# Kernel tuning notes

Measured on AMD Instinct MI355X. Metric: run time of the kernel, lower is better.

## Reference

```python
import jax, jax.numpy as jnp
import numpy as np

D = 1024  # q_dim == k_dim == v_dim
B, QL, KL = 8, 2048, 2048
NEG_BIG = -1e12  # matches torch masked_fill_(-1000000000000.0)


def setup_inputs() -> dict:
    key = jax.random.key(0)
    kq, kk, kv, kp = jax.random.split(key, 4)
    Q = jax.random.normal(kq, (B, QL, D), dtype=jnp.float32)
    K = jax.random.normal(kk, (B, KL, D), dtype=jnp.float32)
    V = jax.random.normal(kv, (B, KL, D), dtype=jnp.float32)
    attn_mask = jnp.zeros((QL, KL), dtype=jnp.float32)
    key_pad_mask = jax.random.randint(kp, (B, KL), 0, 2).astype(jnp.bool_)
    return {"Q": Q, "K": K, "V": V, "attn_mask": attn_mask, "key_pad_mask": key_pad_mask}


def reference(Q, K, V, attn_mask, key_pad_mask):
    temperature = jnp.asarray(np.sqrt(D), dtype=Q.dtype)
    # [B, QL, KL] scores: dot mode
    scores = jnp.einsum("bqd,bkd->bqk", Q, K) / temperature
    scores = scores + attn_mask[None, :, :]
    scores = jnp.where(key_pad_mask[:, None, :], NEG_BIG, scores)
    attn_weights = jax.nn.softmax(scores, axis=-1)  # dropout p=0 -> identity
    attn_ctx = jnp.einsum("bqk,bkd->bqd", attn_weights, V)
    return attn_ctx, attn_weights
```

## Files before the change

kernel.cpp:

```cpp
#include <hip/hip_runtime.h>
#include <hip/hip_fp16.h>

#define B_ 8
#define QL_ 2048
#define KL_ 2048
#define D_ 1024

typedef _Float16 f16x8 __attribute__((ext_vector_type(8)));
typedef _Float16 f16x4 __attribute__((ext_vector_type(4)));
typedef float f32x4 __attribute__((ext_vector_type(4)));

__device__ __forceinline__ void async16(const void* g, void* l) {
  __builtin_amdgcn_global_load_lds(
      (const __attribute__((address_space(1))) unsigned int*)g,
      (__attribute__((address_space(3))) unsigned int*)l, 16, 0, 0);
}

__global__ __launch_bounds__(256) void prep_k(const int* __restrict__ pad,
                                              int* __restrict__ pos,
                                              int* __restrict__ kcp) {
  const int b = blockIdx.x;
  const int t = threadIdx.x;
  const int lane = t & 63, wv = t >> 6;
  __shared__ int wsum[4], wpre[4], kc_sh;
  const int* pr = pad + b * KL_;
  int* po = pos + b * KL_;
  int c[8], loc = 0;
#pragma unroll
  for (int j = 0; j < 8; ++j) {
    c[j] = (pr[t * 8 + j] == 0);
    loc += c[j];
  }
  int inc = loc;
  for (int d = 1; d < 64; d <<= 1) {
    int v = __shfl_up(inc, d);
    if (lane >= d) inc += v;
  }
  if (lane == 63) wsum[wv] = inc;
  __syncthreads();
  if (t == 0) {
    int acc = 0;
    for (int w = 0; w < 4; ++w) {
      wpre[w] = acc;
      acc += wsum[w];
    }
    kc_sh = acc;
    kcp[b] = (acc == 0) ? KL_ : acc;
  }
  __syncthreads();
  const int kc = kc_sh;
  int base = wpre[wv] + inc - loc;
#pragma unroll
  for (int j = 0; j < 8; ++j) {
    po[t * 8 + j] = (kc == 0) ? (t * 8 + j) : base;
    base += c[j];
  }
}

__global__ __launch_bounds__(256) void cvt2_k(const float* __restrict__ Q,
                                              const float* __restrict__ K,
                                              _Float16* __restrict__ Qh,
                                              _Float16* __restrict__ Kh) {
  constexpr int HALF = B_ * QL_ * D_ / 8 / 256;
  const bool isQ = blockIdx.x < HALF;
  const int i = (isQ ? blockIdx.x : blockIdx.x - HALF) * 256 + threadIdx.x;
  const float4* src = reinterpret_cast<const float4*>(isQ ? Q : K);
  const float scale = isQ ? 0.03125f : 1.0f;
  float4 a = src[i * 2], b = src[i * 2 + 1];
  f16x8 h;
  h[0] = (_Float16)(a.x * scale); h[1] = (_Float16)(a.y * scale);
  h[2] = (_Float16)(a.z * scale); h[3] = (_Float16)(a.w * scale);
  h[4] = (_Float16)(b.x * scale); h[5] = (_Float16)(b.y * scale);
  h[6] = (_Float16)(b.z * scale); h[7] = (_Float16)(b.w * scale);
  reinterpret_cast<f16x8*>(isQ ? Qh : Kh)[i] = h;
}

__global__ __launch_bounds__(256) void vt_k(const float* __restrict__ V,
                                            _Float16* __restrict__ VT) {
  __shared__ float tile[32][33];
  const int k0 = blockIdx.x * 32, d0 = blockIdx.y * 32, b = blockIdx.z;
  const float* Vb = V + (size_t)b * KL_ * D_;
  _Float16* VTb = VT + (size_t)b * D_ * KL_;
  const int c = threadIdx.x & 31, r = threadIdx.x >> 5;
#pragma unroll
  for (int s = 0; s < 4; ++s)
    tile[r + s * 8][c] = Vb[(size_t)(k0 + r + s * 8) * D_ + d0 + c];
  __syncthreads();
#pragma unroll
  for (int s = 0; s < 4; ++s)
    VTb[(size_t)(d0 + r + s * 8) * KL_ + k0 + c] = (_Float16)tile[c][r + s * 8];
}

__global__ __launch_bounds__(256) void vtc_k(const float* __restrict__ V,
                                             _Float16* __restrict__ VTc,
                                             const int* __restrict__ pad,
                                             const int* __restrict__ pos) {
  __shared__ float tile[32][33];
  const int k0 = blockIdx.x * 32, d0 = blockIdx.y * 32, b = blockIdx.z;
  const float* Vb = V + (size_t)b * KL_ * D_;
  _Float16* VTb = VTc + (size_t)b * D_ * KL_;
  const int c = threadIdx.x & 31, r = threadIdx.x >> 5;
#pragma unroll
  for (int s = 0; s < 4; ++s)
    tile[r + s * 8][c] = Vb[(size_t)(k0 + r + s * 8) * D_ + d0 + c];
  __syncthreads();
  const int kk = k0 + c;
  const int keep = (pad[b * KL_ + kk] == 0);
  const int col = pos[b * KL_ + kk];
#pragma unroll
  for (int s = 0; s < 4; ++s)
    if (keep)
      VTb[(size_t)(d0 + r + s * 8) * KL_ + col] = (_Float16)tile[c][r + s * 8];
}

template <bool SCORES>
__global__ __launch_bounds__(512, 2) void fgemm_k(
    const _Float16* __restrict__ Ah, const _Float16* __restrict__ Bh,
    float* __restrict__ Cf, _Float16* __restrict__ Ch) {
  constexpr int Mc = 2048;
  constexpr int Nc = SCORES ? 2048 : 1024;
  constexpr int Kc = SCORES ? 1024 : 2048;
  constexpr int NIT = Kc / 64;
  constexpr int GX = Mc / 256, GY = Nc / 256;
  constexpr int CPX = B_ * GX * GY / 8;

  extern __shared__ char lds[];

  const int t = threadIdx.x;
  const int lane = t & 63;
  const int wid = t >> 6;
  const int wr = wid >> 2, wc = wid & 3;
  const int lo = lane & 15, hi = lane >> 4;

  const int id = blockIdx.x;
  const int swz = (id & 7) * CPX + (id >> 3);
  const int b = swz / (GX * GY);
  const int rem = swz % (GX * GY);
  const int m0 = (rem / GY) * 256, n0 = (rem % GY) * 256;

  const _Float16* Ab = Ah + (size_t)b * Mc * Kc;
  const _Float16* Bb = Bh + (size_t)b * Nc * Kc;

  int aoff[4], boff[4], ldst[4];
#pragma unroll
  for (int j = 0; j < 4; ++j) {
    const int row = j * 64 + wid * 8 + (lane >> 3);
    const int cg = (lane & 7) ^ (lane >> 3);
    aoff[j] = (m0 + row) * Kc + cg * 8;
    boff[j] = (n0 + row) * Kc + cg * 8;
    ldst[j] = j * 8192 + wid * 1024;
  }

  auto stage = [&](int it, int slot) {
    char* base = lds + slot * 65536;
    const int kb = it * 64;
#pragma unroll
    for (int j = 0; j < 4; ++j) {
      async16(Ab + aoff[j] + kb, base + ldst[j]);
      async16(Bb + boff[j] + kb, base + 32768 + ldst[j]);
    }
  };

  f32x4 acc[8][4];
#pragma unroll
  for (int m = 0; m < 8; ++m)
#pragma unroll
    for (int n = 0; n < 4; ++n)
#pragma unroll
      for (int i = 0; i < 4; ++i) acc[m][n][i] = 0.0f;

  int raf[8], rbf_[4];
#pragma unroll
  for (int m = 0; m < 8; ++m) {
    const int r = wr * 128 + m * 16 + lo;
    raf[m] = r * 128 + ((hi ^ (r & 7)) << 4);
  }
#pragma unroll
  for (int n = 0; n < 4; ++n) {
    const int r = wc * 64 + n * 16 + lo;
    rbf_[n] = r * 128 + ((hi ^ (r & 7)) << 4);
  }

  auto compute = [&](int slot) {
    const char* Ac = lds + slot * 65536;
    const char* Bc = Ac + 32768;
#pragma unroll
    for (int kh = 0; kh < 2; ++kh) {
      const int kx = kh * 64;
      f16x8 af[8], bfr[4];
#pragma unroll
      for (int m = 0; m < 8; ++m)
        af[m] = *reinterpret_cast<const f16x8*>(Ac + (raf[m] ^ kx));
#pragma unroll
      for (int n = 0; n < 4; ++n)
        bfr[n] = *reinterpret_cast<const f16x8*>(Bc + (rbf_[n] ^ kx));
      __builtin_amdgcn_s_setprio(1);
#pragma unroll
      for (int m = 0; m < 8; ++m)
#pragma unroll
        for (int n = 0; n < 4; ++n)
          acc[m][n] = __builtin_amdgcn_mfma_f32_16x16x32_f16(
              af[m], bfr[n], acc[m][n], 0, 0, 0);
      __builtin_amdgcn_s_setprio(0);
      __builtin_amdgcn_sched_barrier(0);
    }
  };

  stage(0, 0);
  for (int it = 0; it < NIT; ++it) {
    asm volatile("s_waitcnt vmcnt(0) lgkmcnt(0)" ::: "memory");
    __builtin_amdgcn_sched_barrier(0);
    __builtin_amdgcn_s_barrier();
    if (it + 1 < NIT) stage(it + 1, (it + 1) & 1);
    compute(it & 1);
  }

  if constexpr (SCORES) {
    _Float16* Cb = Ch + (size_t)b * Mc * Nc;
#pragma unroll
    for (int n = 0; n < 4; ++n) {
      const int col = n0 + wc * 64 + n * 16 + lo;
#pragma unroll
      for (int m = 0; m < 8; ++m) {
        const int r0 = m0 + wr * 128 + m * 16 + hi * 4;
#pragma unroll
        for (int i = 0; i < 4; ++i)
          Cb[(size_t)(r0 + i) * Nc + col] = (_Float16)acc[m][n][i];
      }
    }
  } else {
    float* Cb = Cf + (size_t)b * Mc * Nc;
#pragma unroll
    for (int n = 0; n < 4; ++n) {
      const int col = n0 + wc * 64 + n * 16 + lo;
#pragma unroll
      for (int m = 0; m < 8; ++m) {
        const int r0 = m0 + wr * 128 + m * 16 + hi * 4;
#pragma unroll
        for (int i = 0; i < 4; ++i)
          Cb[(size_t)(r0 + i) * Nc + col] = acc[m][n][i];
      }
    }
  }
}

__global__ __launch_bounds__(512, 2) void fgemm_pv(
    const _Float16* __restrict__ Whc, const _Float16* __restrict__ VTc,
    float* __restrict__ Cf, const int* __restrict__ kcp) {
  constexpr int Mc = 2048, Nc = 1024;
  constexpr int GX = 8, GY = 4;
  constexpr int CPX = B_ * GX * GY / 8;

  extern __shared__ char lds[];

  const int t = threadIdx.x;
  const int lane = t & 63;
  const int wid = t >> 6;
  const int wr = wid >> 2, wc = wid & 3;
  const int lo = lane & 15, hi = lane >> 4;

  const int id = blockIdx.x;
  const int swz = (id & 7) * CPX + (id >> 3);
  const int b = swz / (GX * GY);
  const int rem = swz % (GX * GY);
  const int m0 = (rem / GY) * 256, n0 = (rem % GY) * 256;

  const int kc = kcp[b];
  const int KA = (kc + 63) & ~63;
  const int NIT = KA >> 6;

  const _Float16* Ab = Whc + (size_t)b * 2048 * 2048;
  const _Float16* Bb = VTc + (size_t)b * Nc * KL_;

  int aoff[4], boff[4], ldst[4];
#pragma unroll
  for (int j = 0; j < 4; ++j) {
    const int row = j * 64 + wid * 8 + (lane >> 3);
    const int cg = (lane & 7) ^ (lane >> 3);
    aoff[j] = (m0 + row) * KA + cg * 8;
    boff[j] = (n0 + row) * KL_ + cg * 8;
    ldst[j] = j * 8192 + wid * 1024;
  }

  auto stage = [&](int it, int slot) {
    char* base = lds + slot * 65536;
    const int kb = it * 64;
#pragma unroll
    for (int j = 0; j < 4; ++j) {
      async16(Ab + aoff[j] + kb, base + ldst[j]);
      async16(Bb + boff[j] + kb, base + 32768 + ldst[j]);
    }
  };

  f32x4 acc[8][4];
#pragma unroll
  for (int m = 0; m < 8; ++m)
#pragma unroll
    for (int n = 0; n < 4; ++n)
#pragma unroll
      for (int i = 0; i < 4; ++i) acc[m][n][i] = 0.0f;

  int raf[8], rbf_[4];
#pragma unroll
  for (int m = 0; m < 8; ++m) {
    const int r = wr * 128 + m * 16 + lo;
    raf[m] = r * 128 + ((hi ^ (r & 7)) << 4);
  }
#pragma unroll
  for (int n = 0; n < 4; ++n) {
    const int r = wc * 64 + n * 16 + lo;
    rbf_[n] = r * 128 + ((hi ^ (r & 7)) << 4);
  }

  auto compute = [&](int slot) {
    const char* Ac = lds + slot * 65536;
    const char* Bc = Ac + 32768;
#pragma unroll
    for (int kh = 0; kh < 2; ++kh) {
      const int kx = kh * 64;
      f16x8 af[8], bfr[4];
#pragma unroll
      for (int m = 0; m < 8; ++m)
        af[m] = *reinterpret_cast<const f16x8*>(Ac + (raf[m] ^ kx));
#pragma unroll
      for (int n = 0; n < 4; ++n)
        bfr[n] = *reinterpret_cast<const f16x8*>(Bc + (rbf_[n] ^ kx));
      __builtin_amdgcn_s_setprio(1);
#pragma unroll
      for (int m = 0; m < 8; ++m)
#pragma unroll
        for (int n = 0; n < 4; ++n)
          acc[m][n] = __builtin_amdgcn_mfma_f32_16x16x32_f16(
              af[m], bfr[n], acc[m][n], 0, 0, 0);
      __builtin_amdgcn_s_setprio(0);
      __builtin_amdgcn_sched_barrier(0);
    }
  };

  stage(0, 0);
  for (int it = 0; it < NIT; ++it) {
    asm volatile("s_waitcnt vmcnt(0) lgkmcnt(0)" ::: "memory");
    __builtin_amdgcn_sched_barrier(0);
    __builtin_amdgcn_s_barrier();
    if (it + 1 < NIT) stage(it + 1, (it + 1) & 1);
    compute(it & 1);
  }

  float* Cb = Cf + (size_t)b * Mc * Nc;
#pragma unroll
  for (int n = 0; n < 4; ++n) {
    const int col = n0 + wc * 64 + n * 16 + lo;
#pragma unroll
    for (int m = 0; m < 8; ++m) {
      const int r0 = m0 + wr * 128 + m * 16 + hi * 4;
#pragma unroll
      for (int i = 0; i < 4; ++i)
        Cb[(size_t)(r0 + i) * Nc + col] = acc[m][n][i];
    }
  }
}

template <bool COMPACT>
__global__ __launch_bounds__(256) void softmax_k(
    const _Float16* __restrict__ Sh, float* __restrict__ W,
    _Float16* __restrict__ Wh, const float* __restrict__ mask,
    const int* __restrict__ pad, const int* __restrict__ pos,
    const int* __restrict__ kcp) {
  const int row = blockIdx.x * 4 + (threadIdx.x >> 6);
  const int lane = threadIdx.x & 63;
  const int b = row >> 11, q = row & 2047;
  const f16x4* Sr = reinterpret_cast<const f16x4*>(Sh + (size_t)row * KL_);
  float4* Wr = reinterpret_cast<float4*>(W + (size_t)row * KL_);
  const float4* Mr = reinterpret_cast<const float4*>(mask + (size_t)q * KL_);
  const int4* Pr = reinterpret_cast<const int4*>(pad + (size_t)b * KL_);
  int4 pk[8];
  float4 v[8];
#pragma unroll
  for (int s = 0; s < 8; ++s) {
    f16x4 sv = Sr[s * 64 + lane];
    float4 mk = Mr[s * 64 + lane];
    int4 p = Pr[s * 64 + lane];
    pk[s] = p;
    float4 x;
    x.x = p.x ? -1e12f : (float)sv[0] + mk.x;
    x.y = p.y ? -1e12f : (float)sv[1] + mk.y;
    x.z = p.z ? -1e12f : (float)sv[2] + mk.z;
    x.w = p.w ? -1e12f : (float)sv[3] + mk.w;
    v[s] = x;
  }
  float mx = -3.402823466e38f;
#pragma unroll
  for (int s = 0; s < 8; ++s)
    mx = fmaxf(mx, fmaxf(fmaxf(v[s].x, v[s].y), fmaxf(v[s].z, v[s].w)));
#pragma unroll
  for (int off = 32; off > 0; off >>= 1) mx = fmaxf(mx, __shfl_xor(mx, off));
  float sum = 0.0f;
#pragma unroll
  for (int s = 0; s < 8; ++s) {
    v[s].x = __expf(v[s].x - mx);
    v[s].y = __expf(v[s].y - mx);
    v[s].z = __expf(v[s].z - mx);
    v[s].w = __expf(v[s].w - mx);
    sum += v[s].x + v[s].y + v[s].z + v[s].w;
  }
#pragma unroll
  for (int off = 32; off > 0; off >>= 1) sum += __shfl_xor(sum, off);
  const float inv = 1.0f / sum;

  if constexpr (COMPACT) {
    const int kc = kcp[b];
    const int kcpad = (kc + 63) & ~63;
    _Float16* Wc = Wh + (size_t)b * 2048 * 2048 + (size_t)q * kcpad;
    const int4* Po = reinterpret_cast<const int4*>(pos + (size_t)b * KL_);
#pragma unroll
    for (int s = 0; s < 8; ++s) {
      float4 o;
      o.x = v[s].x * inv;
      o.y = v[s].y * inv;
      o.z = v[s].z * inv;
      o.w = v[s].w * inv;
      Wr[s * 64 + lane] = o;
      int4 ps = Po[s * 64 + lane];
      if (!pk[s].x) Wc[ps.x] = (_Float16)o.x;
      if (!pk[s].y) Wc[ps.y] = (_Float16)o.y;
      if (!pk[s].z) Wc[ps.z] = (_Float16)o.z;
      if (!pk[s].w) Wc[ps.w] = (_Float16)o.w;
    }
    if (kc + lane < kcpad) Wc[kc + lane] = (_Float16)0.0f;
  } else {
    f16x4* Whr = reinterpret_cast<f16x4*>(Wh + (size_t)row * KL_);
#pragma unroll
    for (int s = 0; s < 8; ++s) {
      float4 o;
      o.x = v[s].x * inv;
      o.y = v[s].y * inv;
      o.z = v[s].z * inv;
      o.w = v[s].w * inv;
      Wr[s * 64 + lane] = o;
      f16x4 h;
      h[0] = (_Float16)o.x;
      h[1] = (_Float16)o.y;
      h[2] = (_Float16)o.z;
      h[3] = (_Float16)o.w;
      Whr[s * 64 + lane] = h;
    }
  }
}

extern "C" void kernel_launch(void* const* d_in, const int* in_sizes, int n_in,
                              void* d_out, int out_size, void* d_ws,
                              size_t ws_size, hipStream_t stream) {
  const float* Q = (const float*)d_in[0];
  const float* K = (const float*)d_in[1];
  const float* V = (const float*)d_in[2];
  const float* mask = (const float*)d_in[3];
  const int* pad = (const int*)d_in[4];

  float* ctx = (float*)d_out;
  float* W = ctx + (size_t)B_ * QL_ * D_;
  _Float16* Sh = (_Float16*)d_out;

  const size_t MB = 1024 * 1024;
  _Float16* VT = (_Float16*)d_ws;
  _Float16* Qh = (_Float16*)((char*)d_ws + 32 * MB);
  _Float16* Kh = (_Float16*)((char*)d_ws + 64 * MB);
  _Float16* Wh = Qh;

  (void)hipFuncSetAttribute((const void*)fgemm_k<true>,
                            hipFuncAttributeMaxDynamicSharedMemorySize, 131072);
  (void)hipFuncSetAttribute((const void*)fgemm_k<false>,
                            hipFuncAttributeMaxDynamicSharedMemorySize, 131072);
  (void)hipFuncSetAttribute((const void*)fgemm_pv,
                            hipFuncAttributeMaxDynamicSharedMemorySize, 131072);

  const bool compact = ws_size >= 96 * MB + (1 << 17);
  if (compact) {
    int* pos = (int*)((char*)d_ws + 96 * MB);
    int* kcp = pos + B_ * KL_;
    prep_k<<<dim3(B_), 256, 0, stream>>>(pad, pos, kcp);
    cvt2_k<<<dim3(2 * B_ * QL_ * D_ / 8 / 256), 256, 0, stream>>>(Q, K, Qh, Kh);
    vtc_k<<<dim3(KL_ / 32, D_ / 32, B_), 256, 0, stream>>>(V, VT, pad, pos);
    fgemm_k<true><<<dim3(B_ * 8 * 8), 512, 131072, stream>>>(Qh, Kh, nullptr,
                                                             Sh);
    softmax_k<true><<<dim3(B_ * QL_ / 4), 256, 0, stream>>>(Sh, W, Wh, mask,
                                                            pad, pos, kcp);
    fgemm_pv<<<dim3(B_ * 8 * 4), 512, 131072, stream>>>(Wh, VT, ctx, kcp);
  } else {
    cvt2_k<<<dim3(2 * B_ * QL_ * D_ / 8 / 256), 256, 0, stream>>>(Q, K, Qh, Kh);
    vt_k<<<dim3(KL_ / 32, D_ / 32, B_), 256, 0, stream>>>(V, VT);
    fgemm_k<true><<<dim3(B_ * 8 * 8), 512, 131072, stream>>>(Qh, Kh, nullptr,
                                                             Sh);
    softmax_k<false><<<dim3(B_ * QL_ / 4), 256, 0, stream>>>(
        Sh, W, Wh, mask, pad, nullptr, nullptr);
    fgemm_k<false><<<dim3(B_ * 8 * 4), 512, 131072, stream>>>(Wh, VT, ctx,
                                                              nullptr);
  }
}
```

Baseline: 249.3 us.

## Compact unpadded K rows and skip padded key tiles in QK GEMM

The float-to-half conversion now writes only the non-padded K rows, packed densely per batch using the prefix-sum positions. A new QK^T GEMM runs over this compacted K, returns early for column tiles beyond the valid key count, and scatters each result column back to its original key index through a new inverse map built in prep_k. The goal is to drop the matmul work on masked keys, which the softmax zeroes out anyway. The cost is indirect scattered column stores, and the padded score columns are left unwritten, so correctness depends on the softmax ignoring them.

```diff
diff --git a/kernel.cpp b/kernel.cpp
--- a/kernel.cpp
+++ b/kernel.cpp
@@ -18,6 +18,7 @@
 
 __global__ __launch_bounds__(256) void prep_k(const int* __restrict__ pad,
                                               int* __restrict__ pos,
+                                              int* __restrict__ inv,
                                               int* __restrict__ kcp) {
   const int b = blockIdx.x;
   const int t = threadIdx.x;
@@ -25,6 +26,7 @@
   __shared__ int wsum[4], wpre[4], kc_sh;
   const int* pr = pad + b * KL_;
   int* po = pos + b * KL_;
+  int* iv = inv + b * KL_;
   int c[8], loc = 0;
 #pragma unroll
   for (int j = 0; j < 8; ++j) {
@@ -52,7 +54,14 @@
   int base = wpre[wv] + inc - loc;
 #pragma unroll
   for (int j = 0; j < 8; ++j) {
-    po[t * 8 + j] = (kc == 0) ? (t * 8 + j) : base;
+    const int k = t * 8 + j;
+    if (kc == 0) {
+      po[k] = k;
+      iv[k] = k;
+    } else {
+      po[k] = base;
+      if (c[j]) iv[base] = k;
+    }
     base += c[j];
   }
 }
@@ -75,6 +84,36 @@
   reinterpret_cast<f16x8*>(isQ ? Qh : Kh)[i] = h;
 }
 
+__global__ __launch_bounds__(256) void cvt2c_k(const float* __restrict__ Q,
+                                               const float* __restrict__ K,
+                                               _Float16* __restrict__ Qh,
+                                               _Float16* __restrict__ Khc,
+                                               const int* __restrict__ pad,
+                                               const int* __restrict__ pos) {
+  constexpr int HALF = B_ * QL_ * D_ / 8 / 256;
+  const bool isQ = blockIdx.x < HALF;
+  const int i = (isQ ? blockIdx.x : blockIdx.x - HALF) * 256 + threadIdx.x;
+  const float4* src = reinterpret_cast<const float4*>(isQ ? Q : K);
+  const float scale = isQ ? 0.03125f : 1.0f;
+  float4 a = src[i * 2], b = src[i * 2 + 1];
+  f16x8 h;
+  h[0] = (_Float16)(a.x * scale); h[1] = (_Float16)(a.y * scale);
+  h[2] = (_Float16)(a.z * scale); h[3] = (_Float16)(a.w * scale);
+  h[4] = (_Float16)(b.x * scale); h[5] = (_Float16)(b.y * scale);
+  h[6] = (_Float16)(b.z * scale); h[7] = (_Float16)(b.w * scale);
+  if (isQ) {
+    reinterpret_cast<f16x8*>(Qh)[i] = h;
+  } else {
+    const int gk = (i * 8) >> 10;
+    const int col8 = i & 127;
+    if (pad[gk] == 0) {
+      const int b = gk >> 11;
+      const int prow = pos[gk];
+      reinterpret_cast<f16x8*>(Khc)[(size_t)(b << 11 | prow) * 128 + col8] = h;
+    }
+  }
+}
+
 __global__ __launch_bounds__(256) void vt_k(const float* __restrict__ V,
                                             _Float16* __restrict__ VT) {
   __shared__ float tile[32][33];
@@ -239,6 +278,127 @@
 #pragma unroll
         for (int i = 0; i < 4; ++i)
           Cb[(size_t)(r0 + i) * Nc + col] = acc[m][n][i];
+      }
+    }
+  }
+}
+
+__global__ __launch_bounds__(512, 2) void fgemm_qkc(
+    const _Float16* __restrict__ Qh, const _Float16* __restrict__ Khc,
+    _Float16* __restrict__ Sh, const int* __restrict__ inv,
+    const int* __restrict__ kcp) {
+  constexpr int Mc = 2048, Nc = 2048, Kc = 1024;
+  constexpr int NIT = Kc / 64;
+  constexpr int GX = 8, GY = 8;
+  constexpr int CPX = B_ * GX * GY / 8;
+
+  extern __shared__ char lds[];
+
+  const int t = threadIdx.x;
+  const int lane = t & 63;
+  const int wid = t >> 6;
+  const int wr = wid >> 2, wc = wid & 3;
+  const int lo = lane & 15, hi = lane >> 4;
+
+  const int id = blockIdx.x;
+  const int swz = (id & 7) * CPX + (id >> 3);
+  const int b = swz / (GX * GY);
+  const int rem = swz % (GX * GY);
+  const int m0 = (rem / GY) * 256, n0 = (rem % GY) * 256;
+
+  const int kc = kcp[b];
+  if (n0 >= ((kc + 63) & ~63)) return;
+
+  const _Float16* Ab = Qh + (size_t)b * Mc * Kc;
+  const _Float16* Bb = Khc + (size_t)b * Nc * Kc;
+
+  int aoff[4], boff[4], ldst[4];
+#pragma unroll
+  for (int j = 0; j < 4; ++j) {
+    const int row = j * 64 + wid * 8 + (lane >> 3);
+    const int cg = (lane & 7) ^ (lane >> 3);
+    aoff[j] = (m0 + row) * Kc + cg * 8;
+    boff[j] = (n0 + row) * Kc + cg * 8;
+    ldst[j] = j * 8192 + wid * 1024;
+  }
+
+  auto stage = [&](int it, int slot) {
+    char* base = lds + slot * 65536;
+    const int kb = it * 64;
+#pragma unroll
+    for (int j = 0; j < 4; ++j) {
+      async16(Ab + aoff[j] + kb, base + ldst[j]);
+      async16(Bb + boff[j] + kb, base + 32768 + ldst[j]);
+    }
+  };
+
+  f32x4 acc[8][4];
+#pragma unroll
+  for (int m = 0; m < 8; ++m)
+#pragma unroll
+    for (int n = 0; n < 4; ++n)
+#pragma unroll
+      for (int i = 0; i < 4; ++i) acc[m][n][i] = 0.0f;
+
+  int raf[8], rbf_[4];
+#pragma unroll
+  for (int m = 0; m < 8; ++m) {
+    const int r = wr * 128 + m * 16 + lo;
+    raf[m] = r * 128 + ((hi ^ (r & 7)) << 4);
+  }
+#pragma unroll
+  for (int n = 0; n < 4; ++n) {
+    const int r = wc * 64 + n * 16 + lo;
+    rbf_[n] = r * 128 + ((hi ^ (r & 7)) << 4);
+  }
+
+  auto compute = [&](int slot) {
+    const char* Ac = lds + slot * 65536;
+    const char* Bc = Ac + 32768;
+#pragma unroll
+    for (int kh = 0; kh < 2; ++kh) {
+      const int kx = kh * 64;
+      f16x8 af[8], bfr[4];
+#pragma unroll
+      for (int m = 0; m < 8; ++m)
+        af[m] = *reinterpret_cast<const f16x8*>(Ac + (raf[m] ^ kx));
+#pragma unroll
+      for (int n = 0; n < 4; ++n)
+        bfr[n] = *reinterpret_cast<const f16x8*>(Bc + (rbf_[n] ^ kx));
+      __builtin_amdgcn_s_setprio(1);
+#pragma unroll
+      for (int m = 0; m < 8; ++m)
+#pragma unroll
+        for (int n = 0; n < 4; ++n)
+          acc[m][n] = __builtin_amdgcn_mfma_f32_16x16x32_f16(
+              af[m], bfr[n], acc[m][n], 0, 0, 0);
+      __builtin_amdgcn_s_setprio(0);
+      __builtin_amdgcn_sched_barrier(0);
+    }
+  };
+
+  stage(0, 0);
+  for (int it = 0; it < NIT; ++it) {
+    asm volatile("s_waitcnt vmcnt(0) lgkmcnt(0)" ::: "memory");
+    __builtin_amdgcn_sched_barrier(0);
+    __builtin_amdgcn_s_barrier();
+    if (it + 1 < NIT) stage(it + 1, (it + 1) & 1);
+    compute(it & 1);
+  }
+
+  _Float16* Cb = Sh + (size_t)b * Mc * Nc;
+  const int* ivb = inv + b * KL_;
+#pragma unroll
+  for (int n = 0; n < 4; ++n) {
+    const int ccol = n0 + wc * 64 + n * 16 + lo;
+    if (ccol < kc) {
+      const int dcol = ivb[ccol];
+#pragma unroll
+      for (int m = 0; m < 8; ++m) {
+        const int r0 = m0 + wr * 128 + m * 16 + hi * 4;
+#pragma unroll
+        for (int i = 0; i < 4; ++i)
+          Cb[(size_t)(r0 + i) * Nc + dcol] = (_Float16)acc[m][n][i];
       }
     }
   }
@@ -470,18 +630,21 @@
                             hipFuncAttributeMaxDynamicSharedMemorySize, 131072);
   (void)hipFuncSetAttribute((const void*)fgemm_k<false>,
                             hipFuncAttributeMaxDynamicSharedMemorySize, 131072);
+  (void)hipFuncSetAttribute((const void*)fgemm_qkc,
+                            hipFuncAttributeMaxDynamicSharedMemorySize, 131072);
   (void)hipFuncSetAttribute((const void*)fgemm_pv,
                             hipFuncAttributeMaxDynamicSharedMemorySize, 131072);
 
-  const bool compact = ws_size >= 96 * MB + (1 << 17);
+  const bool compact = ws_size >= 96 * MB + (1 << 18);
   if (compact) {
     int* pos = (int*)((char*)d_ws + 96 * MB);
-    int* kcp = pos + B_ * KL_;
-    prep_k<<<dim3(B_), 256, 0, stream>>>(pad, pos, kcp);
-    cvt2_k<<<dim3(2 * B_ * QL_ * D_ / 8 / 256), 256, 0, stream>>>(Q, K, Qh, Kh);
+    int* inv = pos + B_ * KL_;
+    int* kcp = inv + B_ * KL_;
+    prep_k<<<dim3(B_), 256, 0, stream>>>(pad, pos, inv, kcp);
+    cvt2c_k<<<dim3(2 * B_ * QL_ * D_ / 8 / 256), 256, 0, stream>>>(
+        Q, K, Qh, Kh, pad, pos);
     vtc_k<<<dim3(KL_ / 32, D_ / 32, B_), 256, 0, stream>>>(V, VT, pad, pos);
-    fgemm_k<true><<<dim3(B_ * 8 * 8), 512, 131072, stream>>>(Qh, Kh, nullptr,
-                                                             Sh);
+    fgemm_qkc<<<dim3(B_ * 8 * 8), 512, 131072, stream>>>(Qh, Kh, Sh, inv, kcp);
     softmax_k<true><<<dim3(B_ * QL_ / 4), 256, 0, stream>>>(Sh, W, Wh, mask,
                                                             pad, pos, kcp);
     fgemm_pv<<<dim3(B_ * 8 * 4), 512, 131072, stream>>>(Wh, VT, ctx, kcp);
```

New measurement: 252.0 us. About the same (+1.1%).
